# Kernel optimization log

Hardware: AMD Instinct MI355X
Metric: run time of the kernel (lower is better)

The kernel has to match this reference:

```python
import jax, jax.numpy as jnp
import numpy as np

N = 262144
FC = 256
XYZ_FREQ, DIR_FREQ = 10, 4
IN_XYZ = 3 + 3 * 2 * XYZ_FREQ  # 63
IN_DIR = 3 + 3 * 2 * DIR_FREQ  # 27
SKIP = 4


def posenc(p, n_freqs):
    bands = 2.0 ** jnp.arange(n_freqs, dtype=p.dtype)          # [F]
    xb = p[..., None, :] * bands[:, None]                       # [N, F, 3]
    sc = jnp.stack([jnp.sin(xb), jnp.cos(xb)], axis=-2)         # [N, F, 2, 3]
    return jnp.concatenate([p, sc.reshape(p.shape[0], n_freqs * 6)], axis=-1)


def setup_inputs() -> dict:
    key = jax.random.key(0)
    ks = jax.random.split(key, 32)
    s = 0.05
    inp = {"x": jax.random.normal(ks[0], (N, 6), jnp.float32)}
    dims_in = [IN_XYZ] + [FC + IN_XYZ if i == SKIP else FC for i in range(1, 8)]
    for i in range(8):
        inp[f"w{i}"] = jax.random.normal(ks[1 + i], (dims_in[i], FC), jnp.float32) * s
        inp[f"b{i}"] = jnp.zeros((FC,), jnp.float32)
    inp["w_final"] = jax.random.normal(ks[10], (FC, FC), jnp.float32) * s
    inp["b_final"] = jnp.zeros((FC,), jnp.float32)
    inp["w_sigma"] = jax.random.normal(ks[11], (FC, 1), jnp.float32) * s
    inp["b_sigma"] = jnp.zeros((1,), jnp.float32)
    inp["w_rgb1"] = jax.random.normal(ks[12], (FC + IN_DIR, FC // 2), jnp.float32) * s
    inp["b_rgb1"] = jnp.zeros((FC // 2,), jnp.float32)
    inp["w_rgb2"] = jax.random.normal(ks[13], (FC // 2, 3), jnp.float32) * s
    inp["b_rgb2"] = jnp.zeros((3,), jnp.float32)
    return inp


def reference(x, w0, b0, w1, b1, w2, b2, w3, b3, w4, b4, w5, b5, w6, b6, w7, b7,
              w_final, b_final, w_sigma, b_sigma, w_rgb1, b_rgb1, w_rgb2, b_rgb2):
    input_xyz = posenc(x[:, :3], XYZ_FREQ)   # [N, 63]
    input_dir = posenc(x[:, 3:], DIR_FREQ)   # [N, 27]
    ws = [w0, w1, w2, w3, w4, w5, w6, w7]
    bs = [b0, b1, b2, b3, b4, b5, b6, b7]
    h = input_xyz
    for i in range(8):
        if i == SKIP:
            h = jnp.concatenate([input_xyz, h], axis=-1)
        h = jax.nn.relu(h @ ws[i] + bs[i])
    sigma = h @ w_sigma + b_sigma                               # [N, 1]
    final = h @ w_final + b_final                               # [N, 256]
    dir_enc = jnp.concatenate([final, input_dir], axis=-1)      # [N, 283]
    hidden = jax.nn.relu(dir_enc @ w_rgb1 + b_rgb1)
    rgb = jax.nn.sigmoid(hidden @ w_rgb2 + b_rgb2)              # [N, 3]
    return jnp.concatenate([rgb, sigma], axis=-1)               # [N, 4]
```

## Files before the change

kernel.cpp:

```cpp
#include <hip/hip_runtime.h>
#include <hip/hip_fp16.h>
#include <stdint.h>

typedef unsigned int   uint32;
typedef unsigned short ushort_t;
typedef _Float16 half8   __attribute__((ext_vector_type(8)));
typedef float    floatx4 __attribute__((ext_vector_type(4)));

#define DEVINL __device__ __forceinline__

#define HSTR 264
#define XSTR 72
#define DSTR 40
#define N_FRAGS 1172

__device__ __align__(16) ushort_t g_ws[(size_t)N_FRAGS * 512];

DEVINL ushort_t f2h_u(float v) { return __half_as_ushort(__float2half(v)); }

DEVINL uint4 make_frag_qword(const float* __restrict__ W, int Kr, int Nr,
                             int skip63, int kt, int nt, int q, int cc)
{
    const int n = nt*16 + cc;
    uint32 pk[4];
    #pragma unroll
    for (int jj = 0; jj < 4; ++jj) {
        ushort_t h2[2];
        #pragma unroll
        for (int e = 0; e < 2; ++e) {
            const int k = kt*32 + q*8 + jj*2 + e;
            float v = 0.f;
            if (n < Nr) {
                if (skip63) {
                    if (k != 63) { const int rr = (k < 63) ? k : (k - 1); v = W[(size_t)rr*Nr + n]; }
                } else if (k < Kr) {
                    v = W[(size_t)k*Nr + n];
                }
            }
            h2[e] = f2h_u(v);
        }
        pk[jj] = (uint32)h2[0] | ((uint32)h2[1] << 16);
    }
    return make_uint4(pk[0], pk[1], pk[2], pk[3]);
}

__global__ __launch_bounds__(256) void prep_weights(
    const float* __restrict__ w0, const float* __restrict__ w1,
    const float* __restrict__ w2, const float* __restrict__ w3,
    const float* __restrict__ w4, const float* __restrict__ w5,
    const float* __restrict__ w6, const float* __restrict__ w7,
    const float* __restrict__ wf, const float* __restrict__ wsig,
    const float* __restrict__ wr1, const float* __restrict__ wr2)
{
    int gid  = blockIdx.x * 256 + threadIdx.x;
    int frag = gid >> 6;
    if (frag >= N_FRAGS) return;
    int lane = gid & 63;
    const int foff[13] = {0,32,160,288,416,576,704,832,960,1088,1096,1168,1172};
    const int NT[12]   = {16,16,16,16,16,16,16,16,16,1,8,1};
    const int KR[12]   = {63,256,256,256,319,256,256,256,256,256,283,128};
    const int NR[12]   = {256,256,256,256,256,256,256,256,256,1,128,3};
    const float* WP[12] = {w0,w1,w2,w3,w4,w5,w6,w7,wf,wsig,wr1,wr2};
    int t = 0;
    while (frag >= foff[t+1]) ++t;
    int fl = frag - foff[t];
    int nt = fl % NT[t];
    int kt = fl / NT[t];
    uint4 pk = make_frag_qword(WP[t], KR[t], NR[t], (t == 4) ? 1 : 0, kt, nt,
                               lane >> 4, lane & 15);
    *(uint4*)(g_ws + (size_t)frag*512 + lane*8) = pk;
}

template <int NT_W, int KT, int KT_SPLIT, int NTT>
DEVINL void run_layer(const ushort_t* __restrict__ wsrc,
                      const ushort_t* in0, int s0,
                      const ushort_t* in1, int s1,
                      int lane, int q, int cc, int nt_lo,
                      floatx4 (&acc)[4][NT_W])
{
    const floatx4 vzero = {0.f, 0.f, 0.f, 0.f};
    #pragma unroll
    for (int rt = 0; rt < 4; ++rt)
        #pragma unroll
        for (int nt = 0; nt < NT_W; ++nt)
            acc[rt][nt] = vzero;

    half8 bfr[2][4];
    half8 afr[2][NT_W];

    auto loadk = [&](int kt, int buf) {
        const ushort_t* src; int st, kk;
        if (kt < KT_SPLIT) { src = in0; st = s0; kk = kt*32; }
        else               { src = in1; st = s1; kk = (kt - KT_SPLIT)*32; }
        #pragma unroll
        for (int rt = 0; rt < 4; ++rt)
            bfr[buf][rt] = *(const half8*)(src + (rt*16 + cc)*st + kk + q*8);
        const ushort_t* wb = wsrc + (size_t)(kt*NTT + nt_lo)*512 + lane*8;
        #pragma unroll
        for (int nt = 0; nt < NT_W; ++nt)
            afr[buf][nt] = *(const half8*)(wb + nt*512);
    };

    loadk(0, 0);
    #pragma unroll
    for (int kt = 0; kt < KT; ++kt) {
        const int cur = kt & 1;
        if (kt + 1 < KT) loadk(kt + 1, cur ^ 1);
        #pragma unroll
        for (int nt = 0; nt < NT_W; ++nt)
            #pragma unroll
            for (int rt = 0; rt < 4; ++rt)
                acc[rt][nt] = __builtin_amdgcn_mfma_f32_16x16x32_f16(
                    afr[cur][nt], bfr[cur][rt], acc[rt][nt], 0, 0, 0);
    }
}

template <int NT_W, bool RELU>
DEVINL void epilogue_h(floatx4 (&acc)[4][NT_W], const float* __restrict__ bias,
                       int nt_lo, ushort_t* shh, int q, int cc)
{
    #pragma unroll
    for (int rt = 0; rt < 4; ++rt) {
        const int m = rt*16 + cc;
        #pragma unroll
        for (int nt = 0; nt < NT_W; ++nt) {
            const int n = (nt_lo + nt)*16 + q*4;
            floatx4 v = acc[rt][nt];
            const floatx4 bb = *(const floatx4*)(bias + n);
            v = v + bb;
            if (RELU) {
                v.x = fmaxf(v.x, 0.f); v.y = fmaxf(v.y, 0.f);
                v.z = fmaxf(v.z, 0.f); v.w = fmaxf(v.w, 0.f);
            }
            uint2 u;
            u.x = (uint32)f2h_u(v.x) | ((uint32)f2h_u(v.y) << 16);
            u.y = (uint32)f2h_u(v.z) | ((uint32)f2h_u(v.w) << 16);
            *(uint2*)(shh + (size_t)m*HSTR + n) = u;
        }
    }
}

__global__ __launch_bounds__(256, 2) void nerf_fused(
    const float* __restrict__ x,
    const float* __restrict__ b0, const float* __restrict__ b1,
    const float* __restrict__ b2, const float* __restrict__ b3,
    const float* __restrict__ b4, const float* __restrict__ b5,
    const float* __restrict__ b6, const float* __restrict__ b7,
    const float* __restrict__ bf, const float* __restrict__ bsig,
    const float* __restrict__ br1, const float* __restrict__ br2,
    float* __restrict__ out)
{
    __shared__ __align__(16) ushort_t shh[64*HSTR];
    __shared__ __align__(16) ushort_t shx[64*XSTR];
    __shared__ __align__(16) ushort_t shd[64*DSTR];

    const int tid  = threadIdx.x;
    const int wave = tid >> 6, lane = tid & 63;
    const int q = lane >> 4, cc = lane & 15;
    const int r0 = blockIdx.x * 64;
    const ushort_t* ws = g_ws;

    {
        const int r = lane;
        const float* xr = x + (size_t)(r0 + r)*6;
        for (int j = wave; j < 42; j += 4) {
            if (j < 30) {
                int f = j/3, a = j%3;
                float v = xr[a] * (float)(1 << f);
                shx[r*XSTR + 3 + f*6 + a]     = f2h_u(sinf(v));
                shx[r*XSTR + 3 + f*6 + 3 + a] = f2h_u(cosf(v));
            } else {
                int jj = j - 30, f = jj/3, a = jj%3;
                float v = xr[3+a] * (float)(1 << f);
                shd[r*DSTR + 3 + f*6 + a]     = f2h_u(sinf(v));
                shd[r*DSTR + 3 + f*6 + 3 + a] = f2h_u(cosf(v));
            }
        }
        if (wave == 0) {
            #pragma unroll
            for (int a = 0; a < 3; ++a) {
                shx[r*XSTR + a] = f2h_u(xr[a]);
                shd[r*DSTR + a] = f2h_u(xr[3+a]);
            }
            shx[r*XSTR + 63] = 0;
            #pragma unroll
            for (int kq = 27; kq < 32; ++kq) shd[r*DSTR + kq] = 0;
        }
    }
    __syncthreads();

    const float* BS[8] = {b0,b1,b2,b3,b4,b5,b6,b7};
    const int WO[8] = {0,16384,81920,147456,212992,294912,360448,425984};
    const int nt_lo4 = wave * 4;

    floatx4 acc[4][4];

    run_layer<4,2,2,16>(ws + WO[0], shx, XSTR, shx, XSTR, lane, q, cc, nt_lo4, acc);
    epilogue_h<4,true>(acc, b0, nt_lo4, shh, q, cc);
    __syncthreads();

    #pragma unroll
    for (int l = 1; l < 8; ++l) {
        if (l == 4)
            run_layer<4,10,2,16>(ws + WO[4], shx, XSTR, shh, HSTR, lane, q, cc, nt_lo4, acc);
        else
            run_layer<4,8,8,16>(ws + WO[l], shh, HSTR, shh, HSTR, lane, q, cc, nt_lo4, acc);
        __syncthreads();
        epilogue_h<4,true>(acc, BS[l], nt_lo4, shh, q, cc);
        __syncthreads();
    }

    if (wave == 0) {
        floatx4 sacc[4][1];
        run_layer<1,8,8,1>(ws + 557056, shh, HSTR, shh, HSTR, lane, q, cc, 0, sacc);
        if (q == 0) {
            const float bs_ = bsig[0];
            #pragma unroll
            for (int rt = 0; rt < 4; ++rt)
                out[(size_t)(r0 + rt*16 + cc)*4 + 3] = sacc[rt][0].x + bs_;
        }
    }

    run_layer<4,8,8,16>(ws + 491520, shh, HSTR, shh, HSTR, lane, q, cc, nt_lo4, acc);
    __syncthreads();
    epilogue_h<4,false>(acc, bf, nt_lo4, shh, q, cc);
    __syncthreads();

    {
        floatx4 racc[4][2];
        run_layer<2,9,8,8>(ws + 561152, shh, HSTR, shd, DSTR, lane, q, cc, wave*2, racc);
        __syncthreads();
        epilogue_h<2,true>(racc, br1, wave*2, shh, q, cc);
        __syncthreads();
    }

    if (wave == 0) {
        floatx4 cacc[4][1];
        run_layer<1,4,4,1>(ws + 598016, shh, HSTR, shh, HSTR, lane, q, cc, 0, cacc);
        if (q == 0) {
            const float c0 = br2[0], c1 = br2[1], c2 = br2[2];
            #pragma unroll
            for (int rt = 0; rt < 4; ++rt) {
                const size_t o = (size_t)(r0 + rt*16 + cc)*4;
                out[o+0] = 1.f/(1.f + expf(-(cacc[rt][0].x + c0)));
                out[o+1] = 1.f/(1.f + expf(-(cacc[rt][0].y + c1)));
                out[o+2] = 1.f/(1.f + expf(-(cacc[rt][0].z + c2)));
            }
        }
    }
}

extern "C" void kernel_launch(void* const* d_in, const int* in_sizes, int n_in,
                              void* d_out, int out_size, void* d_ws, size_t ws_size,
                              hipStream_t stream)
{
    const float* x  = (const float*)d_in[0];
    const float* w0 = (const float*)d_in[1];  const float* b0 = (const float*)d_in[2];
    const float* w1 = (const float*)d_in[3];  const float* b1 = (const float*)d_in[4];
    const float* w2 = (const float*)d_in[5];  const float* b2 = (const float*)d_in[6];
    const float* w3 = (const float*)d_in[7];  const float* b3 = (const float*)d_in[8];
    const float* w4 = (const float*)d_in[9];  const float* b4 = (const float*)d_in[10];
    const float* w5 = (const float*)d_in[11]; const float* b5 = (const float*)d_in[12];
    const float* w6 = (const float*)d_in[13]; const float* b6 = (const float*)d_in[14];
    const float* w7 = (const float*)d_in[15]; const float* b7 = (const float*)d_in[16];
    const float* wf = (const float*)d_in[17]; const float* bf = (const float*)d_in[18];
    const float* wsg= (const float*)d_in[19]; const float* bsg= (const float*)d_in[20];
    const float* wr1= (const float*)d_in[21]; const float* br1= (const float*)d_in[22];
    const float* wr2= (const float*)d_in[23]; const float* br2= (const float*)d_in[24];
    float* out = (float*)d_out;
    const int N = in_sizes[0] / 6;

    prep_weights<<<(N_FRAGS*64 + 255)/256, 256, 0, stream>>>(
        w0,w1,w2,w3,w4,w5,w6,w7,wf,wsg,wr1,wr2);
    nerf_fused<<<N/64, 256, 0, stream>>>(
        x, b0,b1,b2,b3,b4,b5,b6,b7, bf,bsg, br1,br2, out);
}
```

Baseline: 389.2 us.

## Switch fused NeRF MLP to 32x32x16 MFMA with XOR-swizzled activation LDS

```diff
diff --git a/kernel.cpp b/kernel.cpp
--- a/kernel.cpp
+++ b/kernel.cpp
@@ -4,31 +4,32 @@
 
 typedef unsigned int   uint32;
 typedef unsigned short ushort_t;
-typedef _Float16 half8   __attribute__((ext_vector_type(8)));
-typedef float    floatx4 __attribute__((ext_vector_type(4)));
+typedef _Float16 half8    __attribute__((ext_vector_type(8)));
+typedef float    floatx4  __attribute__((ext_vector_type(4)));
+typedef float    floatx16 __attribute__((ext_vector_type(16)));
 
 #define DEVINL __device__ __forceinline__
 
-#define HSTR 264
 #define XSTR 72
 #define DSTR 40
-#define N_FRAGS 1172
+#define N_FRAGS 1184
 
 __device__ __align__(16) ushort_t g_ws[(size_t)N_FRAGS * 512];
 
 DEVINL ushort_t f2h_u(float v) { return __half_as_ushort(__float2half(v)); }
 
 DEVINL uint4 make_frag_qword(const float* __restrict__ W, int Kr, int Nr,
-                             int skip63, int kt, int nt, int q, int cc)
-{
-    const int n = nt*16 + cc;
+                             int skip63, int k16, int nt32, int lane)
+{
+    const int n  = nt32*32 + (lane & 31);
+    const int h5 = lane >> 5;
     uint32 pk[4];
     #pragma unroll
     for (int jj = 0; jj < 4; ++jj) {
         ushort_t h2[2];
         #pragma unroll
         for (int e = 0; e < 2; ++e) {
-            const int k = kt*32 + q*8 + jj*2 + e;
+            const int k = k16*16 + h5*8 + jj*2 + e;
             float v = 0.f;
             if (n < Nr) {
                 if (skip63) {
@@ -56,86 +57,97 @@
     int frag = gid >> 6;
     if (frag >= N_FRAGS) return;
     int lane = gid & 63;
-    const int foff[13] = {0,32,160,288,416,576,704,832,960,1088,1096,1168,1172};
-    const int NT[12]   = {16,16,16,16,16,16,16,16,16,1,8,1};
-    const int KR[12]   = {63,256,256,256,319,256,256,256,256,256,283,128};
-    const int NR[12]   = {256,256,256,256,256,256,256,256,256,1,128,3};
+    const int foff[13]  = {0,32,160,288,416,576,704,832,960,1088,1104,1176,1184};
+    const int NT32[12]  = {8,8,8,8,8,8,8,8,8,1,4,1};
+    const int KR[12]    = {63,256,256,256,319,256,256,256,256,256,283,128};
+    const int NR[12]    = {256,256,256,256,256,256,256,256,256,1,128,3};
     const float* WP[12] = {w0,w1,w2,w3,w4,w5,w6,w7,wf,wsig,wr1,wr2};
     int t = 0;
     while (frag >= foff[t+1]) ++t;
-    int fl = frag - foff[t];
-    int nt = fl % NT[t];
-    int kt = fl / NT[t];
-    uint4 pk = make_frag_qword(WP[t], KR[t], NR[t], (t == 4) ? 1 : 0, kt, nt,
-                               lane >> 4, lane & 15);
+    int fl   = frag - foff[t];
+    int nt32 = fl % NT32[t];
+    int k16  = fl / NT32[t];
+    uint4 pk = make_frag_qword(WP[t], KR[t], NR[t], (t == 4) ? 1 : 0, k16, nt32, lane);
     *(uint4*)(g_ws + (size_t)frag*512 + lane*8) = pk;
 }
 
-template <int NT_W, int KT, int KT_SPLIT, int NTT>
-DEVINL void run_layer(const ushort_t* __restrict__ wsrc,
-                      const ushort_t* in0, int s0,
-                      const ushort_t* in1, int s1,
-                      int lane, int q, int cc, int nt_lo,
-                      floatx4 (&acc)[4][NT_W])
-{
-    const floatx4 vzero = {0.f, 0.f, 0.f, 0.f};
-    #pragma unroll
-    for (int rt = 0; rt < 4; ++rt)
-        #pragma unroll
-        for (int nt = 0; nt < NT_W; ++nt)
-            acc[rt][nt] = vzero;
-
-    half8 bfr[2][4];
-    half8 afr[2][NT_W];
-
-    auto loadk = [&](int kt, int buf) {
-        const ushort_t* src; int st, kk;
-        if (kt < KT_SPLIT) { src = in0; st = s0; kk = kt*32; }
-        else               { src = in1; st = s1; kk = (kt - KT_SPLIT)*32; }
-        #pragma unroll
-        for (int rt = 0; rt < 4; ++rt)
-            bfr[buf][rt] = *(const half8*)(src + (rt*16 + cc)*st + kk + q*8);
-        const ushort_t* wb = wsrc + (size_t)(kt*NTT + nt_lo)*512 + lane*8;
-        #pragma unroll
-        for (int nt = 0; nt < NT_W; ++nt)
-            afr[buf][nt] = *(const half8*)(wb + nt*512);
+template <int NFT, int K16T, int K16_SPLIT, int NTT32, bool SWZ0, bool SWZ1>
+DEVINL void run_layer32(const ushort_t* __restrict__ wsrc,
+                        const ushort_t* in0, int s0,
+                        const ushort_t* in1, int s1,
+                        int lane, int nt_lo32,
+                        floatx16 (&acc)[2][NFT])
+{
+    const floatx16 vz = {0,0,0,0,0,0,0,0,0,0,0,0,0,0,0,0};
+    #pragma unroll
+    for (int rt2 = 0; rt2 < 2; ++rt2)
+        #pragma unroll
+        for (int ft = 0; ft < NFT; ++ft)
+            acc[rt2][ft] = vz;
+
+    const int ml = lane & 31, h5 = lane >> 5;
+    half8 afr[2][NFT], bfr[2][2];
+
+    auto loadk = [&](int k16, int buf) {
+        const ushort_t* src; int st; bool swz; int kk;
+        if (k16 < K16_SPLIT) { src = in0; st = s0; swz = SWZ0; kk = k16; }
+        else                 { src = in1; st = s1; swz = SWZ1; kk = k16 - K16_SPLIT; }
+        #pragma unroll
+        for (int rt2 = 0; rt2 < 2; ++rt2) {
+            const int m = rt2*32 + ml;
+            const ushort_t* p = swz
+                ? src + m*256 + (((kk*2 + h5) ^ (m & 7)) * 8)
+                : src + m*st + kk*16 + h5*8;
+            bfr[buf][rt2] = *(const half8*)p;
+        }
+        const ushort_t* wb = wsrc + (size_t)(k16*NTT32 + nt_lo32)*512 + lane*8;
+        #pragma unroll
+        for (int ft = 0; ft < NFT; ++ft)
+            afr[buf][ft] = *(const half8*)(wb + ft*512);
     };
 
     loadk(0, 0);
     #pragma unroll
-    for (int kt = 0; kt < KT; ++kt) {
-        const int cur = kt & 1;
-        if (kt + 1 < KT) loadk(kt + 1, cur ^ 1);
-        #pragma unroll
-        for (int nt = 0; nt < NT_W; ++nt)
-            #pragma unroll
-            for (int rt = 0; rt < 4; ++rt)
-                acc[rt][nt] = __builtin_amdgcn_mfma_f32_16x16x32_f16(
-                    afr[cur][nt], bfr[cur][rt], acc[rt][nt], 0, 0, 0);
-    }
-}
-
-template <int NT_W, bool RELU>
-DEVINL void epilogue_h(floatx4 (&acc)[4][NT_W], const float* __restrict__ bias,
-                       int nt_lo, ushort_t* shh, int q, int cc)
-{
-    #pragma unroll
-    for (int rt = 0; rt < 4; ++rt) {
-        const int m = rt*16 + cc;
-        #pragma unroll
-        for (int nt = 0; nt < NT_W; ++nt) {
-            const int n = (nt_lo + nt)*16 + q*4;
-            floatx4 v = acc[rt][nt];
-            const floatx4 bb = *(const floatx4*)(bias + n);
-            v = v + bb;
-            if (RELU) {
-                v.x = fmaxf(v.x, 0.f); v.y = fmaxf(v.y, 0.f);
-                v.z = fmaxf(v.z, 0.f); v.w = fmaxf(v.w, 0.f);
-            }
-            uint2 u;
-            u.x = (uint32)f2h_u(v.x) | ((uint32)f2h_u(v.y) << 16);
-            u.y = (uint32)f2h_u(v.z) | ((uint32)f2h_u(v.w) << 16);
-            *(uint2*)(shh + (size_t)m*HSTR + n) = u;
+    for (int k16 = 0; k16 < K16T; ++k16) {
+        const int cur = k16 & 1;
+        if (k16 + 1 < K16T) loadk(k16 + 1, cur ^ 1);
+        #pragma unroll
+        for (int ft = 0; ft < NFT; ++ft)
+            #pragma unroll
+            for (int rt2 = 0; rt2 < 2; ++rt2)
+                acc[rt2][ft] = __builtin_amdgcn_mfma_f32_32x32x16_f16(
+                    afr[cur][ft], bfr[cur][rt2], acc[rt2][ft], 0, 0, 0);
+    }
+}
+
+template <int NFT, bool RELU>
+DEVINL void epi32(floatx16 (&acc)[2][NFT], const float* __restrict__ bias,
+                  int nt_lo32, ushort_t* __restrict__ shh, int lane)
+{
+    const int ml = lane & 31, h5 = lane >> 5;
+    #pragma unroll
+    for (int rt2 = 0; rt2 < 2; ++rt2) {
+        const int m = rt2*32 + ml;
+        #pragma unroll
+        for (int ft = 0; ft < NFT; ++ft) {
+            #pragma unroll
+            for (int g = 0; g < 4; ++g) {
+                const int n = (nt_lo32 + ft)*32 + g*8 + h5*4;
+                const floatx4 bb = *(const floatx4*)(bias + n);
+                float v0 = acc[rt2][ft][g*4+0] + bb.x;
+                float v1 = acc[rt2][ft][g*4+1] + bb.y;
+                float v2 = acc[rt2][ft][g*4+2] + bb.z;
+                float v3 = acc[rt2][ft][g*4+3] + bb.w;
+                if (RELU) {
+                    v0 = fmaxf(v0, 0.f); v1 = fmaxf(v1, 0.f);
+                    v2 = fmaxf(v2, 0.f); v3 = fmaxf(v3, 0.f);
+                }
+                uint2 u;
+                u.x = (uint32)f2h_u(v0) | ((uint32)f2h_u(v1) << 16);
+                u.y = (uint32)f2h_u(v2) | ((uint32)f2h_u(v3) << 16);
+                const int chunk = n >> 3;
+                *(uint2*)(shh + m*256 + ((chunk ^ (m & 7)) * 8) + (n & 7)) = u;
+            }
         }
     }
 }
@@ -150,13 +162,13 @@
     const float* __restrict__ br1, const float* __restrict__ br2,
     float* __restrict__ out)
 {
-    __shared__ __align__(16) ushort_t shh[64*HSTR];
+    __shared__ __align__(16) ushort_t shh[64*256];
     __shared__ __align__(16) ushort_t shx[64*XSTR];
     __shared__ __align__(16) ushort_t shd[64*DSTR];
 
     const int tid  = threadIdx.x;
     const int wave = tid >> 6, lane = tid & 63;
-    const int q = lane >> 4, cc = lane & 15;
+    const int ml = lane & 31, h5 = lane >> 5;
     const int r0 = blockIdx.x * 64;
     const ushort_t* ws = g_ws;
 
@@ -191,60 +203,60 @@
 
     const float* BS[8] = {b0,b1,b2,b3,b4,b5,b6,b7};
     const int WO[8] = {0,16384,81920,147456,212992,294912,360448,425984};
-    const int nt_lo4 = wave * 4;
-
-    floatx4 acc[4][4];
-
-    run_layer<4,2,2,16>(ws + WO[0], shx, XSTR, shx, XSTR, lane, q, cc, nt_lo4, acc);
-    epilogue_h<4,true>(acc, b0, nt_lo4, shh, q, cc);
+    const int ntl = wave * 2;
+
+    floatx16 acc[2][2];
+
+    run_layer32<2,4,4,8,false,false>(ws + WO[0], shx, XSTR, shx, XSTR, lane, ntl, acc);
+    epi32<2,true>(acc, b0, ntl, shh, lane);
     __syncthreads();
 
     #pragma unroll
     for (int l = 1; l < 8; ++l) {
         if (l == 4)
-            run_layer<4,10,2,16>(ws + WO[4], shx, XSTR, shh, HSTR, lane, q, cc, nt_lo4, acc);
+            run_layer32<2,20,4,8,false,true>(ws + WO[4], shx, XSTR, shh, 256, lane, ntl, acc);
         else
-            run_layer<4,8,8,16>(ws + WO[l], shh, HSTR, shh, HSTR, lane, q, cc, nt_lo4, acc);
-        __syncthreads();
-        epilogue_h<4,true>(acc, BS[l], nt_lo4, shh, q, cc);
+            run_layer32<2,16,16,8,true,true>(ws + WO[l], shh, 256, shh, 256, lane, ntl, acc);
+        __syncthreads();
+        epi32<2,true>(acc, BS[l], ntl, shh, lane);
         __syncthreads();
     }
 
     if (wave == 0) {
-        floatx4 sacc[4][1];
-        run_layer<1,8,8,1>(ws + 557056, shh, HSTR, shh, HSTR, lane, q, cc, 0, sacc);
-        if (q == 0) {
+        floatx16 sacc[2][1];
+        run_layer32<1,16,16,1,true,true>(ws + 557056, shh, 256, shh, 256, lane, 0, sacc);
+        if (h5 == 0) {
             const float bs_ = bsig[0];
             #pragma unroll
-            for (int rt = 0; rt < 4; ++rt)
-                out[(size_t)(r0 + rt*16 + cc)*4 + 3] = sacc[rt][0].x + bs_;
-        }
-    }
-
-    run_layer<4,8,8,16>(ws + 491520, shh, HSTR, shh, HSTR, lane, q, cc, nt_lo4, acc);
-    __syncthreads();
-    epilogue_h<4,false>(acc, bf, nt_lo4, shh, q, cc);
+            for (int rt2 = 0; rt2 < 2; ++rt2)
+                out[(size_t)(r0 + rt2*32 + ml)*4 + 3] = sacc[rt2][0][0] + bs_;
+        }
+    }
+
+    run_layer32<2,16,16,8,true,true>(ws + 491520, shh, 256, shh, 256, lane, ntl, acc);
+    __syncthreads();
+    epi32<2,false>(acc, bf, ntl, shh, lane);
     __syncthreads();
 
     {
-        floatx4 racc[4][2];
-        run_layer<2,9,8,8>(ws + 561152, shh, HSTR, shd, DSTR, lane, q, cc, wave*2, racc);
-        __syncthreads();
-        epilogue_h<2,true>(racc, br1, wave*2, shh, q, cc);
+        floatx16 racc[2][1];
+        run_layer32<1,18,16,4,true,false>(ws + 565248, shh, 256, shd, DSTR, lane, wave, racc);
+        __syncthreads();
+        epi32<1,true>(racc, br1, wave, shh, lane);
         __syncthreads();
     }
 
     if (wave == 0) {
-        floatx4 cacc[4][1];
-        run_layer<1,4,4,1>(ws + 598016, shh, HSTR, shh, HSTR, lane, q, cc, 0, cacc);
-        if (q == 0) {
+        floatx16 cacc[2][1];
+        run_layer32<1,8,8,1,true,true>(ws + 602112, shh, 256, shh, 256, lane, 0, cacc);
+        if (h5 == 0) {
             const float c0 = br2[0], c1 = br2[1], c2 = br2[2];
             #pragma unroll
-            for (int rt = 0; rt < 4; ++rt) {
-                const size_t o = (size_t)(r0 + rt*16 + cc)*4;
-                out[o+0] = 1.f/(1.f + expf(-(cacc[rt][0].x + c0)));
-                out[o+1] = 1.f/(1.f + expf(-(cacc[rt][0].y + c1)));
-                out[o+2] = 1.f/(1.f + expf(-(cacc[rt][0].z + c2)));
+            for (int rt2 = 0; rt2 < 2; ++rt2) {
+                const size_t o = (size_t)(r0 + rt2*32 + ml)*4;
+                out[o+0] = 1.f/(1.f + expf(-(cacc[rt2][0][0] + c0)));
+                out[o+1] = 1.f/(1.f + expf(-(cacc[rt2][0][1] + c1)));
+                out[o+2] = 1.f/(1.f + expf(-(cacc[rt2][0][2] + c2)));
             }
         }
     }
```

New measurement: 489.6 us. +25.8%, slower.
